# Performance work log

Measured on AMD Instinct MI355X. Metric: run time of the kernel, lower is better.

Reference implementation:

```python
import jax, jax.numpy as jnp
import numpy as np

V, E, H, S = 32000, 1024, 1024, 2048


def setup_inputs() -> dict:
    key = jax.random.key(0)
    ks = jax.random.split(key, 16)
    std = 0.02
    return {
        "encoder_out": jax.random.normal(ks[0], (S, E), jnp.float32),
        "word_input": jax.random.randint(ks[1], (1,), 0, V, jnp.int32),
        "last_context": jax.random.normal(ks[2], (1, H), jnp.float32),
        "h0": jnp.zeros((1, 1, H), jnp.float32),
        "c0": jnp.zeros((1, 1, H), jnp.float32),
        # learned parameters
        "emb": jax.random.normal(ks[3], (V, E), jnp.float32) * std,
        "W_ih": jax.random.normal(ks[4], (4 * H, E + H), jnp.float32) * std,
        "W_hh": jax.random.normal(ks[5], (4 * H, H), jnp.float32) * std,
        "b_ih": jnp.zeros((4 * H,), jnp.float32),
        "b_hh": jnp.zeros((4 * H,), jnp.float32),
        "W_attn": jax.random.normal(ks[6], (H, E + H), jnp.float32) * std,
        "b_attn": jnp.zeros((H,), jnp.float32),
        "v": jax.random.uniform(ks[7], (H,), jnp.float32) * 0.1,
        "W_ah": jax.random.normal(ks[8], (H, E + H), jnp.float32) * std,
        "b_ah": jnp.zeros((H,), jnp.float32),
        "W_out": jax.random.normal(ks[9], (V, H), jnp.float32) * std,
        "b_out": jnp.zeros((V,), jnp.float32),
    }


def reference(encoder_out, word_input, last_context, h0, c0,
              emb, W_ih, W_hh, b_ih, b_hh,
              W_attn, b_attn, v, W_ah, b_ah, W_out, b_out):
    # single decoder step, batch=1 (dropout in eval mode == identity)
    embedded = emb[word_input[0]]                       # [E]
    x = jnp.concatenate([last_context[0], embedded])    # [H+E] (context first, as in torch.cat)
    # LSTM cell (PyTorch gate order i, f, g, o)
    gates = W_ih @ x + b_ih + W_hh @ h0[0, 0] + b_hh    # [4H]
    i, f, g, o = jnp.split(gates, 4)
    c = jax.nn.sigmoid(f) * c0[0, 0] + jax.nn.sigmoid(i) * jnp.tanh(g)
    ht = jax.nn.sigmoid(o) * jnp.tanh(c)                # [H]
    # additive attention, vectorized over encoder steps.
    # original concatenates (ht, encoder_out[i]); split attn weight accordingly.
    Wa_h, Wa_e = W_attn[:, :H], W_attn[:, H:]
    scores = jnp.tanh(encoder_out @ Wa_e.T + (Wa_h @ ht + b_attn)) @ v  # [S]
    w = jax.nn.softmax(scores)                          # [S]
    context = w @ encoder_out                           # [E]
    ht_tilda = jnp.tanh(W_ah @ jnp.concatenate([context, ht]) + b_ah)  # [H]
    output = jax.nn.log_softmax(W_out @ ht_tilda + b_out)              # [V]
    return (output[None, :], (ht[None, None, :], c[None, None, :]),
            ht_tilda[None, :], w[None, :])
```

## Files before the change

### kernel.cpp

```cpp
#include <hip/hip_runtime.h>
#include <math.h>

#define V_ 32000
#define E_ 1024
#define H_ 1024
#define S_ 2048

typedef __attribute__((ext_vector_type(8))) short bf16x8;
typedef __attribute__((ext_vector_type(8))) unsigned short u16x8;
typedef __attribute__((ext_vector_type(4))) float f32x4;

typedef __attribute__((address_space(1))) const unsigned int gu32;
typedef __attribute__((address_space(3))) unsigned int lu32;

__device__ __forceinline__ float sigmoidf_(float x) { return 1.0f / (1.0f + expf(-x)); }

__device__ __forceinline__ unsigned short f2bf(float f) {
    unsigned int u = __builtin_bit_cast(unsigned int, f);
    unsigned int r = (u + 0x7fffu + ((u >> 16) & 1u)) >> 16;
    return (unsigned short)r;
}
__device__ __forceinline__ float bf2f(unsigned short u) {
    return __builtin_bit_cast(float, ((unsigned int)u) << 16);
}
__device__ __forceinline__ u16x8 pack8(float4 a, float4 b) {
    u16x8 p;
    p[0] = f2bf(a.x); p[1] = f2bf(a.y); p[2] = f2bf(a.z); p[3] = f2bf(a.w);
    p[4] = f2bf(b.x); p[5] = f2bf(b.y); p[6] = f2bf(b.z); p[7] = f2bf(b.w);
    return p;
}
__device__ __forceinline__ void gload16(const void* g, void* l) {
    __builtin_amdgcn_global_load_lds((gu32*)g, (lu32*)l, 16, 0, 0);
}

__global__ __launch_bounds__(256) void kA(
    const float* __restrict__ W_ih, const float* __restrict__ W_hh,
    const float* __restrict__ b_ih, const float* __restrict__ b_hh,
    const float* __restrict__ last_context, const float* __restrict__ emb,
    const int* __restrict__ word, const float* __restrict__ h0,
    const float* __restrict__ c0, const float* __restrict__ enc,
    const float* __restrict__ W_attn,
    float* __restrict__ out_ht, float* __restrict__ out_c,
    float* __restrict__ ws_ht, unsigned short* __restrict__ encb,
    unsigned short* __restrict__ wab, float* __restrict__ ws_ctx)
{
    int b = blockIdx.x, tid = threadIdx.x;
    int wave = tid >> 6, lane = tid & 63;
    if (b < 1024) {
        __shared__ float sbuf[4];
        int j = b;
        const float* embrow = emb + (size_t)word[0] * E_;
        int row = j + wave * H_;
        const float* wi = W_ih + (size_t)row * (E_ + H_);
        const float* wh = W_hh + (size_t)row * H_;
        float acc = 0.f;
        #pragma unroll
        for (int it = 0; it < 8; ++it) {
            int idx = (lane + it * 64) * 4;
            float4 wv = *(const float4*)(wi + idx);
            float4 xv = (idx < H_) ? *(const float4*)(last_context + idx)
                                   : *(const float4*)(embrow + (idx - H_));
            acc = fmaf(wv.x, xv.x, acc); acc = fmaf(wv.y, xv.y, acc);
            acc = fmaf(wv.z, xv.z, acc); acc = fmaf(wv.w, xv.w, acc);
        }
        {
            float4 hvv[4];
            int nz = 0;
            #pragma unroll
            for (int it = 0; it < 4; ++it) {
                hvv[it] = *(const float4*)(h0 + (lane + it * 64) * 4);
                nz |= (hvv[it].x != 0.f) | (hvv[it].y != 0.f) |
                      (hvv[it].z != 0.f) | (hvv[it].w != 0.f);
            }
            if (__any(nz)) {
                #pragma unroll
                for (int it = 0; it < 4; ++it) {
                    int idx = (lane + it * 64) * 4;
                    float4 wv = *(const float4*)(wh + idx);
                    acc = fmaf(wv.x, hvv[it].x, acc); acc = fmaf(wv.y, hvv[it].y, acc);
                    acc = fmaf(wv.z, hvv[it].z, acc); acc = fmaf(wv.w, hvv[it].w, acc);
                }
            }
        }
        #pragma unroll
        for (int m = 32; m; m >>= 1) acc += __shfl_down(acc, m, 64);
        if (lane == 0) sbuf[wave] = acc;
        __syncthreads();
        if (tid == 0) {
            float gi = sbuf[0] + b_ih[j]          + b_hh[j];
            float gf = sbuf[1] + b_ih[j + H_]     + b_hh[j + H_];
            float gg = sbuf[2] + b_ih[j + 2*H_]   + b_hh[j + 2*H_];
            float go = sbuf[3] + b_ih[j + 3*H_]   + b_hh[j + 3*H_];
            float c  = sigmoidf_(gf) * c0[j] + sigmoidf_(gi) * tanhf(gg);
            float ht = sigmoidf_(go) * tanhf(c);
            out_c[j]  = c;
            out_ht[j] = ht;
            ws_ht[j]  = ht;
        }
        if (b == 0) {
            #pragma unroll
            for (int i = 0; i < 16; ++i)
                ws_ctx[tid + i * 256] = 0.f;
        }
    } else {
        int cid = (b - 1024) * 256 + tid;
        const int ENC_CH = (S_ * E_) / 8;
        #pragma unroll
        for (int i = 0; i < 3; ++i) {
            int idx = cid + i * 131072;
            const float* src;
            unsigned short* dst;
            if (idx < ENC_CH) {
                src = enc + (size_t)idx * 8;
                dst = encb + (size_t)idx * 8;
            } else {
                int w = idx - ENC_CH;
                int h = w >> 7, off = (w & 127) * 8;
                src = W_attn + (size_t)h * (E_ + H_) + H_ + off;
                dst = wab + (size_t)h * E_ + off;
            }
            float4 a = *(const float4*)src;
            float4 bq = *(const float4*)(src + 4);
            *(u16x8*)dst = pack8(a, bq);
        }
    }
}

__global__ __launch_bounds__(256) void kC(
    const float* __restrict__ W_attn, const float* __restrict__ b_attn,
    const float* __restrict__ ws_ht,
    const unsigned short* __restrict__ encb, const unsigned short* __restrict__ wab,
    const float* __restrict__ v, float* __restrict__ spart)
{
    __shared__ unsigned short As[2][64 * 64];
    __shared__ unsigned short Bs[2][64 * 64];
    __shared__ float qsh[64], vsh[64];
    int bx = blockIdx.x, by = blockIdx.y;
    int s0 = bx * 64, h0 = by * 64;
    int tid = threadIdx.x;
    int wave = tid >> 6, lane = tid & 63;

    int r0 = tid >> 3, p0 = tid & 7;
    int lc = (p0 ^ (r0 & 7)) * 8;
    const unsigned short* aS0 = encb + (size_t)(s0 + r0) * E_ + lc;
    const unsigned short* aS1 = encb + (size_t)(s0 + 32 + r0) * E_ + lc;
    const unsigned short* bS0 = wab  + (size_t)(h0 + r0) * E_ + lc;
    const unsigned short* bS1 = wab  + (size_t)(h0 + 32 + r0) * E_ + lc;

    gload16(aS0, As[0] + tid * 8);
    gload16(aS1, As[0] + (tid + 256) * 8);
    gload16(bS0, Bs[0] + tid * 8);
    gload16(bS1, Bs[0] + (tid + 256) * 8);

    {
        float4 hv[4];
        #pragma unroll
        for (int it = 0; it < 4; ++it)
            hv[it] = *(const float4*)(ws_ht + (lane + it * 64) * 4);
        #pragma unroll 1
        for (int bq = 0; bq < 4; ++bq) {
            int rbase = h0 + wave * 16 + bq * 4;
            float qa[4];
            #pragma unroll
            for (int rr = 0; rr < 4; ++rr) {
                const float* rowp = W_attn + (size_t)(rbase + rr) * (E_ + H_);
                float a = 0.f;
                #pragma unroll
                for (int it = 0; it < 4; ++it) {
                    float4 wv = *(const float4*)(rowp + (lane + it * 64) * 4);
                    a = fmaf(wv.x, hv[it].x, a); a = fmaf(wv.y, hv[it].y, a);
                    a = fmaf(wv.z, hv[it].z, a); a = fmaf(wv.w, hv[it].w, a);
                }
                qa[rr] = a;
            }
            #pragma unroll
            for (int rr = 0; rr < 4; ++rr) {
                #pragma unroll
                for (int m = 32; m; m >>= 1) qa[rr] += __shfl_down(qa[rr], m, 64);
            }
            if (lane == 0) {
                #pragma unroll
                for (int rr = 0; rr < 4; ++rr)
                    qsh[wave * 16 + bq * 4 + rr] = qa[rr] + b_attn[rbase + rr];
            }
        }
    }
    if (tid < 64) vsh[tid] = v[h0 + tid];

    int wr = (wave >> 1) * 32, wc = (wave & 1) * 32;
    int fc = lane & 15, g = lane >> 4;
    int aRow[2], bRow[2], pc[2];
    #pragma unroll
    for (int m = 0; m < 2; ++m) aRow[m] = (wr + m * 16 + fc) * 64;
    #pragma unroll
    for (int n = 0; n < 2; ++n) bRow[n] = (wc + n * 16 + fc) * 64;
    #pragma unroll
    for (int kk = 0; kk < 2; ++kk) pc[kk] = ((kk * 4 + g) ^ (fc & 7)) * 8;

    f32x4 acc[2][2];
    #pragma unroll
    for (int m = 0; m < 2; ++m)
        #pragma unroll
        for (int n = 0; n < 2; ++n)
            acc[m][n] = (f32x4){0.f, 0.f, 0.f, 0.f};

    __syncthreads();
    int cur = 0;
    #pragma unroll 1
    for (int t = 0; t < 16; ++t) {
        if (t < 15) {
            int k0 = (t + 1) * 64;
            gload16(aS0 + k0, As[cur ^ 1] + tid * 8);
            gload16(aS1 + k0, As[cur ^ 1] + (tid + 256) * 8);
            gload16(bS0 + k0, Bs[cur ^ 1] + tid * 8);
            gload16(bS1 + k0, Bs[cur ^ 1] + (tid + 256) * 8);
        }
        #pragma unroll
        for (int kk = 0; kk < 2; ++kk) {
            bf16x8 af[2], bf2[2];
            #pragma unroll
            for (int m = 0; m < 2; ++m) af[m] = *(const bf16x8*)(As[cur] + aRow[m] + pc[kk]);
            #pragma unroll
            for (int n = 0; n < 2; ++n) bf2[n] = *(const bf16x8*)(Bs[cur] + bRow[n] + pc[kk]);
            #pragma unroll
            for (int m = 0; m < 2; ++m)
                #pragma unroll
                for (int n = 0; n < 2; ++n)
                    acc[m][n] = __builtin_amdgcn_mfma_f32_16x16x32_bf16(
                        af[m], bf2[n], acc[m][n], 0, 0, 0);
        }
        __syncthreads();
        cur ^= 1;
    }

    float qv[2], vv[2];
    #pragma unroll
    for (int n = 0; n < 2; ++n) {
        int col = wc + n * 16 + fc;
        qv[n] = qsh[col];
        vv[n] = vsh[col];
    }
    int part = by * 2 + (wave & 1);
    #pragma unroll
    for (int m = 0; m < 2; ++m) {
        #pragma unroll
        for (int j = 0; j < 4; ++j) {
            float p = 0.f;
            #pragma unroll
            for (int n = 0; n < 2; ++n)
                p += tanhf(acc[m][n][j] + qv[n]) * vv[n];
            #pragma unroll
            for (int mask = 8; mask; mask >>= 1) p += __shfl_xor(p, mask, 64);
            if (fc == 0)
                spart[(size_t)(s0 + wr + m * 16 + g * 4 + j) * 32 + part] = p;
        }
    }
}

__global__ __launch_bounds__(256) void kD(
    const float* __restrict__ spart, const unsigned short* __restrict__ encb,
    float* __restrict__ expw, float* __restrict__ gpart, float* __restrict__ ctx)
{
    __shared__ float esh[16];
    int b = blockIdx.x, tid = threadIdx.x;
    int s0 = b * 16;
    int sl = tid >> 4, pp = tid & 15;
    float vsum = spart[(size_t)(s0 + sl) * 32 + pp]
               + spart[(size_t)(s0 + sl) * 32 + pp + 16];
    #pragma unroll
    for (int mask = 8; mask; mask >>= 1) vsum += __shfl_xor(vsum, mask, 64);
    if (pp == 0) {
        float e = expf(vsum);
        expw[s0 + sl] = e;
        esh[sl] = e;
    }
    __syncthreads();
    if (tid == 0) {
        float bs = 0.f;
        #pragma unroll
        for (int i = 0; i < 16; ++i) bs += esh[i];
        gpart[b] = bs;
    }
    int e0 = tid * 4;
    float a0 = 0.f, a1 = 0.f, a2 = 0.f, a3 = 0.f;
    #pragma unroll
    for (int ss = 0; ss < 16; ++ss) {
        ushort4 u = *(const ushort4*)(encb + (size_t)(s0 + ss) * E_ + e0);
        float w = esh[ss];
        a0 = fmaf(w, bf2f(u.x), a0);
        a1 = fmaf(w, bf2f(u.y), a1);
        a2 = fmaf(w, bf2f(u.z), a2);
        a3 = fmaf(w, bf2f(u.w), a3);
    }
    float* cdst = ctx + (b & 3) * 1024;
    atomicAdd(&cdst[e0 + 0], a0);
    atomicAdd(&cdst[e0 + 1], a1);
    atomicAdd(&cdst[e0 + 2], a2);
    atomicAdd(&cdst[e0 + 3], a3);
}

__global__ __launch_bounds__(256) void kE(
    const float* __restrict__ W_ah, const float* __restrict__ b_ah,
    const float* __restrict__ ctx, const float* __restrict__ ht,
    const float* __restrict__ gpart, const float* __restrict__ expw,
    float* __restrict__ out_htt, float* __restrict__ ws_htt,
    float* __restrict__ out_w)
{
    int b = blockIdx.x;
    int wave = threadIdx.x >> 6, lane = threadIdx.x & 63;
    float gsum = gpart[lane] + gpart[lane + 64];
    #pragma unroll
    for (int m = 32; m; m >>= 1) gsum += __shfl_xor(gsum, m, 64);
    float invS = 1.0f / gsum;
    if (b >= 256) {
        int s = (b - 256) * 1024 + (int)threadIdx.x * 4;
        float4 e4 = *(const float4*)(expw + s);
        float4 w4 = { e4.x * invS, e4.y * invS, e4.z * invS, e4.w * invS };
        *(float4*)(out_w + s) = w4;
        return;
    }
    int r = b * 4 + wave;
    const float* row = W_ah + (size_t)r * (E_ + H_);
    float acc = 0.f;
    #pragma unroll
    for (int it = 0; it < 8; ++it) {
        int idx = (lane + it * 64) * 4;
        float4 wv = *(const float4*)(row + idx);
        float4 xv;
        if (idx < E_) {
            float4 c0v = *(const float4*)(ctx + idx);
            float4 c1v = *(const float4*)(ctx + 1024 + idx);
            float4 c2v = *(const float4*)(ctx + 2048 + idx);
            float4 c3v = *(const float4*)(ctx + 3072 + idx);
            xv = (float4){ (c0v.x + c1v.x + c2v.x + c3v.x) * invS,
                           (c0v.y + c1v.y + c2v.y + c3v.y) * invS,
                           (c0v.z + c1v.z + c2v.z + c3v.z) * invS,
                           (c0v.w + c1v.w + c2v.w + c3v.w) * invS };
        } else {
            xv = *(const float4*)(ht + idx - E_);
        }
        acc = fmaf(wv.x, xv.x, acc); acc = fmaf(wv.y, xv.y, acc);
        acc = fmaf(wv.z, xv.z, acc); acc = fmaf(wv.w, xv.w, acc);
    }
    #pragma unroll
    for (int m = 32; m; m >>= 1) acc += __shfl_down(acc, m, 64);
    if (lane == 0) {
        float val = tanhf(acc + b_ah[r]);
        out_htt[r] = val;
        ws_htt[r]  = val;
    }
}

__global__ __launch_bounds__(256) void kF(
    const float* __restrict__ W_out, const float* __restrict__ b_out,
    const float* __restrict__ ht_tilda, float* __restrict__ logits,
    float* __restrict__ lpart)
{
    __shared__ float wes[4];
    int b = blockIdx.x;
    int wave = threadIdx.x >> 6, lane = threadIdx.x & 63;
    int r0 = b * 16 + wave * 4;
    const float* w0 = W_out + (size_t)r0 * H_;
    const float* w1 = W_out + (size_t)(r0 + 1) * H_;
    const float* w2 = W_out + (size_t)(r0 + 2) * H_;
    const float* w3 = W_out + (size_t)(r0 + 3) * H_;
    float a0 = 0.f, a1 = 0.f, a2 = 0.f, a3 = 0.f;
    #pragma unroll
    for (int it = 0; it < 4; ++it) {
        int idx = (lane + it * 64) * 4;
        float4 hv = *(const float4*)(ht_tilda + idx);
        float4 v0 = *(const float4*)(w0 + idx);
        float4 v1 = *(const float4*)(w1 + idx);
        float4 v2 = *(const float4*)(w2 + idx);
        float4 v3 = *(const float4*)(w3 + idx);
        a0 = fmaf(v0.x, hv.x, a0); a0 = fmaf(v0.y, hv.y, a0);
        a0 = fmaf(v0.z, hv.z, a0); a0 = fmaf(v0.w, hv.w, a0);
        a1 = fmaf(v1.x, hv.x, a1); a1 = fmaf(v1.y, hv.y, a1);
        a1 = fmaf(v1.z, hv.z, a1); a1 = fmaf(v1.w, hv.w, a1);
        a2 = fmaf(v2.x, hv.x, a2); a2 = fmaf(v2.y, hv.y, a2);
        a2 = fmaf(v2.z, hv.z, a2); a2 = fmaf(v2.w, hv.w, a2);
        a3 = fmaf(v3.x, hv.x, a3); a3 = fmaf(v3.y, hv.y, a3);
        a3 = fmaf(v3.z, hv.z, a3); a3 = fmaf(v3.w, hv.w, a3);
    }
    #pragma unroll
    for (int m = 32; m; m >>= 1) {
        a0 += __shfl_down(a0, m, 64); a1 += __shfl_down(a1, m, 64);
        a2 += __shfl_down(a2, m, 64); a3 += __shfl_down(a3, m, 64);
    }
    if (lane == 0) {
        float lg0 = a0 + b_out[r0];
        float lg1 = a1 + b_out[r0 + 1];
        float lg2 = a2 + b_out[r0 + 2];
        float lg3 = a3 + b_out[r0 + 3];
        logits[r0]     = lg0;
        logits[r0 + 1] = lg1;
        logits[r0 + 2] = lg2;
        logits[r0 + 3] = lg3;
        wes[wave] = expf(lg0) + expf(lg1) + expf(lg2) + expf(lg3);
    }
    __syncthreads();
    if (threadIdx.x == 0)
        lpart[b] = wes[0] + wes[1] + wes[2] + wes[3];
}

__global__ __launch_bounds__(1024) void kG(
    float* __restrict__ out, const float* __restrict__ lpart)
{
    __shared__ float sred[16];
    int b = blockIdx.x, tid = threadIdx.x;
    float s = 0.f;
    #pragma unroll
    for (int k = 0; k < 2; ++k) {
        int i = tid + k * 1024;
        if (i < 2000) s += lpart[i];
    }
    #pragma unroll
    for (int m = 32; m; m >>= 1) s += __shfl_down(s, m, 64);
    if ((tid & 63) == 0) sred[tid >> 6] = s;
    __syncthreads();
    float tot = 0.f;
    #pragma unroll
    for (int i = 0; i < 16; ++i) tot += sred[i];
    float lse = logf(tot);
    #pragma unroll
    for (int k = 0; k < 4; ++k) {
        int row = b * 4000 + k * 1024 + tid;
        if (row < (b + 1) * 4000 && row < V_) out[row] -= lse;
    }
}

extern "C" void kernel_launch(void* const* d_in, const int* in_sizes, int n_in,
                              void* d_out, int out_size, void* d_ws, size_t ws_size,
                              hipStream_t stream) {
    const float* enc          = (const float*)d_in[0];
    const int*   word         = (const int*)  d_in[1];
    const float* last_context = (const float*)d_in[2];
    const float* h0           = (const float*)d_in[3];
    const float* c0           = (const float*)d_in[4];
    const float* emb          = (const float*)d_in[5];
    const float* W_ih         = (const float*)d_in[6];
    const float* W_hh         = (const float*)d_in[7];
    const float* b_ih         = (const float*)d_in[8];
    const float* b_hh         = (const float*)d_in[9];
    const float* W_attn       = (const float*)d_in[10];
    const float* b_attn       = (const float*)d_in[11];
    const float* v            = (const float*)d_in[12];
    const float* W_ah         = (const float*)d_in[13];
    const float* b_ah         = (const float*)d_in[14];
    const float* W_out        = (const float*)d_in[15];
    const float* b_out        = (const float*)d_in[16];

    float* out        = (float*)d_out;
    float* out_logits = out;
    float* out_ht     = out + V_;
    float* out_c      = out + V_ + H_;
    float* out_htt    = out + V_ + 2 * H_;
    float* out_w      = out + V_ + 3 * H_;

    float* ws      = (float*)d_ws;
    float* ws_ht   = ws;
    float* ws_expw = ws + 1024;
    float* ws_ctx  = ws + 3072;
    float* ws_gp   = ws + 7168;
    float* ws_htt  = ws + 7296;
    float* ws_lp   = ws + 8320;
    float* ws_sp   = ws + 16384;
    unsigned short* encb = (unsigned short*)(ws + 81920);
    unsigned short* wab  = encb + (size_t)S_ * E_;

    kA<<<1536, 256, 0, stream>>>(W_ih, W_hh, b_ih, b_hh, last_context, emb, word,
                                 h0, c0, enc, W_attn, out_ht, out_c, ws_ht,
                                 encb, wab, ws_ctx);
    kC<<<dim3(32, 16), 256, 0, stream>>>(W_attn, b_attn, ws_ht, encb, wab, v, ws_sp);
    kD<<<128, 256, 0, stream>>>(ws_sp, encb, ws_expw, ws_gp, ws_ctx);
    kE<<<258, 256, 0, stream>>>(W_ah, b_ah, ws_ctx, ws_ht, ws_gp, ws_expw,
                                out_htt, ws_htt, out_w);
    kF<<<2000, 256, 0, stream>>>(W_out, b_out, ws_htt, out_logits, ws_lp);
    kG<<<8, 1024, 0, stream>>>(out_logits, ws_lp);
}
```

Before: 75.42 us.

## Overlap W_ah hidden-half GEMV with attention GEMM and rebalance reduction kernels

```diff
diff --git a/kernel.cpp b/kernel.cpp
--- a/kernel.cpp
+++ b/kernel.cpp
@@ -99,7 +99,7 @@
         }
         if (b == 0) {
             #pragma unroll
-            for (int i = 0; i < 16; ++i)
+            for (int i = 0; i < 32; ++i)
                 ws_ctx[tid + i * 256] = 0.f;
         }
     } else {
@@ -130,15 +130,38 @@
     const float* __restrict__ W_attn, const float* __restrict__ b_attn,
     const float* __restrict__ ws_ht,
     const unsigned short* __restrict__ encb, const unsigned short* __restrict__ wab,
-    const float* __restrict__ v, float* __restrict__ spart)
+    const float* __restrict__ v, float* __restrict__ spart,
+    const float* __restrict__ W_ah, const float* __restrict__ b_ah,
+    float* __restrict__ hpart)
 {
     __shared__ unsigned short As[2][64 * 64];
     __shared__ unsigned short Bs[2][64 * 64];
     __shared__ float qsh[64], vsh[64];
-    int bx = blockIdx.x, by = blockIdx.y;
-    int s0 = bx * 64, h0 = by * 64;
+    int b = blockIdx.x;
     int tid = threadIdx.x;
     int wave = tid >> 6, lane = tid & 63;
+
+    if (b >= 512) {
+        int r = (b - 512) * 4 + wave;
+        const float* rowp = W_ah + (size_t)r * (E_ + H_) + E_;
+        float acc = 0.f;
+        #pragma unroll
+        for (int it = 0; it < 4; ++it) {
+            int idx = (lane + it * 64) * 4;
+            float4 wv = *(const float4*)(rowp + idx);
+            float4 hv = *(const float4*)(ws_ht + idx);
+            acc = fmaf(wv.x, hv.x, acc); acc = fmaf(wv.y, hv.y, acc);
+            acc = fmaf(wv.z, hv.z, acc); acc = fmaf(wv.w, hv.w, acc);
+        }
+        #pragma unroll
+        for (int m = 32; m; m >>= 1) acc += __shfl_down(acc, m, 64);
+        if (lane == 0) hpart[r] = acc + b_ah[r];
+        return;
+    }
+
+    int by = (b & 7) * 2 + (b >> 8);
+    int bx = (b >> 3) & 31;
+    int s0 = bx * 64, h0 = by * 64;
 
     int r0 = tid >> 3, p0 = tid & 7;
     int lc = (p0 ^ (r0 & 7)) * 8;
@@ -261,14 +284,13 @@
     const float* __restrict__ spart, const unsigned short* __restrict__ encb,
     float* __restrict__ expw, float* __restrict__ gpart, float* __restrict__ ctx)
 {
-    __shared__ float esh[16];
+    __shared__ float esh[8];
     int b = blockIdx.x, tid = threadIdx.x;
-    int s0 = b * 16;
-    int sl = tid >> 4, pp = tid & 15;
-    float vsum = spart[(size_t)(s0 + sl) * 32 + pp]
-               + spart[(size_t)(s0 + sl) * 32 + pp + 16];
-    #pragma unroll
-    for (int mask = 8; mask; mask >>= 1) vsum += __shfl_xor(vsum, mask, 64);
+    int s0 = b * 8;
+    int sl = tid >> 5, pp = tid & 31;
+    float vsum = spart[(size_t)(s0 + sl) * 32 + pp];
+    #pragma unroll
+    for (int mask = 16; mask; mask >>= 1) vsum += __shfl_xor(vsum, mask, 64);
     if (pp == 0) {
         float e = expf(vsum);
         expw[s0 + sl] = e;
@@ -278,13 +300,13 @@
     if (tid == 0) {
         float bs = 0.f;
         #pragma unroll
-        for (int i = 0; i < 16; ++i) bs += esh[i];
+        for (int i = 0; i < 8; ++i) bs += esh[i];
         gpart[b] = bs;
     }
     int e0 = tid * 4;
     float a0 = 0.f, a1 = 0.f, a2 = 0.f, a3 = 0.f;
     #pragma unroll
-    for (int ss = 0; ss < 16; ++ss) {
+    for (int ss = 0; ss < 8; ++ss) {
         ushort4 u = *(const ushort4*)(encb + (size_t)(s0 + ss) * E_ + e0);
         float w = esh[ss];
         a0 = fmaf(w, bf2f(u.x), a0);
@@ -292,7 +314,7 @@
         a2 = fmaf(w, bf2f(u.z), a2);
         a3 = fmaf(w, bf2f(u.w), a3);
     }
-    float* cdst = ctx + (b & 3) * 1024;
+    float* cdst = ctx + (b & 7) * 1024;
     atomicAdd(&cdst[e0 + 0], a0);
     atomicAdd(&cdst[e0 + 1], a1);
     atomicAdd(&cdst[e0 + 2], a2);
@@ -300,15 +322,15 @@
 }
 
 __global__ __launch_bounds__(256) void kE(
-    const float* __restrict__ W_ah, const float* __restrict__ b_ah,
-    const float* __restrict__ ctx, const float* __restrict__ ht,
+    const float* __restrict__ W_ah, const float* __restrict__ ctx,
     const float* __restrict__ gpart, const float* __restrict__ expw,
+    const float* __restrict__ hpart,
     float* __restrict__ out_htt, float* __restrict__ ws_htt,
     float* __restrict__ out_w)
 {
     int b = blockIdx.x;
     int wave = threadIdx.x >> 6, lane = threadIdx.x & 63;
-    float gsum = gpart[lane] + gpart[lane + 64];
+    float gsum = gpart[lane] + gpart[lane + 64] + gpart[lane + 128] + gpart[lane + 192];
     #pragma unroll
     for (int m = 32; m; m >>= 1) gsum += __shfl_xor(gsum, m, 64);
     float invS = 1.0f / gsum;
@@ -323,43 +345,36 @@
     const float* row = W_ah + (size_t)r * (E_ + H_);
     float acc = 0.f;
     #pragma unroll
-    for (int it = 0; it < 8; ++it) {
+    for (int it = 0; it < 4; ++it) {
         int idx = (lane + it * 64) * 4;
         float4 wv = *(const float4*)(row + idx);
-        float4 xv;
-        if (idx < E_) {
-            float4 c0v = *(const float4*)(ctx + idx);
-            float4 c1v = *(const float4*)(ctx + 1024 + idx);
-            float4 c2v = *(const float4*)(ctx + 2048 + idx);
-            float4 c3v = *(const float4*)(ctx + 3072 + idx);
-            xv = (float4){ (c0v.x + c1v.x + c2v.x + c3v.x) * invS,
-                           (c0v.y + c1v.y + c2v.y + c3v.y) * invS,
-                           (c0v.z + c1v.z + c2v.z + c3v.z) * invS,
-                           (c0v.w + c1v.w + c2v.w + c3v.w) * invS };
-        } else {
-            xv = *(const float4*)(ht + idx - E_);
-        }
-        acc = fmaf(wv.x, xv.x, acc); acc = fmaf(wv.y, xv.y, acc);
-        acc = fmaf(wv.z, xv.z, acc); acc = fmaf(wv.w, xv.w, acc);
+        float4 cs = *(const float4*)(ctx + idx);
+        #pragma unroll
+        for (int cp = 1; cp < 8; ++cp) {
+            float4 cv = *(const float4*)(ctx + cp * 1024 + idx);
+            cs.x += cv.x; cs.y += cv.y; cs.z += cv.z; cs.w += cv.w;
+        }
+        acc = fmaf(wv.x, cs.x * invS, acc); acc = fmaf(wv.y, cs.y * invS, acc);
+        acc = fmaf(wv.z, cs.z * invS, acc); acc = fmaf(wv.w, cs.w * invS, acc);
     }
     #pragma unroll
     for (int m = 32; m; m >>= 1) acc += __shfl_down(acc, m, 64);
     if (lane == 0) {
-        float val = tanhf(acc + b_ah[r]);
+        float val = tanhf(acc + hpart[r]);
         out_htt[r] = val;
         ws_htt[r]  = val;
     }
 }
 
-__global__ __launch_bounds__(256) void kF(
+__global__ __launch_bounds__(512) void kF(
     const float* __restrict__ W_out, const float* __restrict__ b_out,
     const float* __restrict__ ht_tilda, float* __restrict__ logits,
     float* __restrict__ lpart)
 {
-    __shared__ float wes[4];
+    __shared__ float wes[8];
     int b = blockIdx.x;
     int wave = threadIdx.x >> 6, lane = threadIdx.x & 63;
-    int r0 = b * 16 + wave * 4;
+    int r0 = b * 32 + wave * 4;
     const float* w0 = W_out + (size_t)r0 * H_;
     const float* w1 = W_out + (size_t)(r0 + 1) * H_;
     const float* w2 = W_out + (size_t)(r0 + 2) * H_;
@@ -399,8 +414,12 @@
         wes[wave] = expf(lg0) + expf(lg1) + expf(lg2) + expf(lg3);
     }
     __syncthreads();
-    if (threadIdx.x == 0)
-        lpart[b] = wes[0] + wes[1] + wes[2] + wes[3];
+    if (threadIdx.x == 0) {
+        float bs = 0.f;
+        #pragma unroll
+        for (int i = 0; i < 8; ++i) bs += wes[i];
+        lpart[b] = bs;
+    }
 }
 
 __global__ __launch_bounds__(1024) void kG(
@@ -408,12 +427,7 @@
 {
     __shared__ float sred[16];
     int b = blockIdx.x, tid = threadIdx.x;
-    float s = 0.f;
-    #pragma unroll
-    for (int k = 0; k < 2; ++k) {
-        int i = tid + k * 1024;
-        if (i < 2000) s += lpart[i];
-    }
+    float s = (tid < 1000) ? lpart[tid] : 0.f;
     #pragma unroll
     for (int m = 32; m; m >>= 1) s += __shfl_down(s, m, 64);
     if ((tid & 63) == 0) sred[tid >> 6] = s;
@@ -461,9 +475,10 @@
     float* ws_ht   = ws;
     float* ws_expw = ws + 1024;
     float* ws_ctx  = ws + 3072;
-    float* ws_gp   = ws + 7168;
-    float* ws_htt  = ws + 7296;
-    float* ws_lp   = ws + 8320;
+    float* ws_gp   = ws + 11264;
+    float* ws_htt  = ws + 11520;
+    float* ws_hp   = ws + 12544;
+    float* ws_lp   = ws + 13568;
     float* ws_sp   = ws + 16384;
     unsigned short* encb = (unsigned short*)(ws + 81920);
     unsigned short* wab  = encb + (size_t)S_ * E_;
@@ -471,10 +486,11 @@
     kA<<<1536, 256, 0, stream>>>(W_ih, W_hh, b_ih, b_hh, last_context, emb, word,
                                  h0, c0, enc, W_attn, out_ht, out_c, ws_ht,
                                  encb, wab, ws_ctx);
-    kC<<<dim3(32, 16), 256, 0, stream>>>(W_attn, b_attn, ws_ht, encb, wab, v, ws_sp);
-    kD<<<128, 256, 0, stream>>>(ws_sp, encb, ws_expw, ws_gp, ws_ctx);
-    kE<<<258, 256, 0, stream>>>(W_ah, b_ah, ws_ctx, ws_ht, ws_gp, ws_expw,
+    kC<<<768, 256, 0, stream>>>(W_attn, b_attn, ws_ht, encb, wab, v, ws_sp,
+                                W_ah, b_ah, ws_hp);
+    kD<<<256, 256, 0, stream>>>(ws_sp, encb, ws_expw, ws_gp, ws_ctx);
+    kE<<<258, 256, 0, stream>>>(W_ah, ws_ctx, ws_gp, ws_expw, ws_hp,
                                 out_htt, ws_htt, out_w);
-    kF<<<2000, 256, 0, stream>>>(W_out, b_out, ws_htt, out_logits, ws_lp);
+    kF<<<1000, 512, 0, stream>>>(W_out, b_out, ws_htt, out_logits, ws_lp);
     kG<<<8, 1024, 0, stream>>>(out_logits, ws_lp);
 }
```

Measured after the change: 78.58 us. 1.04x slower.
